# Kernel tuning notes

Measured on AMD Instinct MI355X. Metric: run time of the kernel, lower is better.

The kernel has to match this reference:

```python
import jax, jax.numpy as jnp
import numpy as np

N_NODES = 50000
N_EDGES = 1000000
NEG_SLOPE = 0.2


def _gat_layer(x, W, attn_l, attn_r, bias, src, dst, n_nodes):
    """DGL-style GATConv. x:[N,Fin], W:[H*D,Fin], attn_l/attn_r:[H,D], bias:[H*D].
    Returns [N, H*D] after ReLU activation (flattened heads)."""
    H, D = attn_l.shape
    h = (x @ W.T).reshape(n_nodes, H, D)                    # [N,H,D]
    el = jnp.sum(h * attn_l[None], axis=-1)                 # [N,H]
    er = jnp.sum(h * attn_r[None], axis=-1)                 # [N,H]
    e = jax.nn.leaky_relu(el[src] + er[dst], NEG_SLOPE)     # [E,H]
    # edge softmax over incoming edges per destination node
    emax = jax.ops.segment_max(e, dst, num_segments=n_nodes)  # [N,H]
    emax = jnp.where(jnp.isfinite(emax), emax, 0.0)
    a = jnp.exp(e - emax[dst])                               # [E,H]
    denom = jax.ops.segment_sum(a, dst, num_segments=n_nodes)  # [N,H]
    alpha = a / denom[dst]                                   # [E,H]
    msg = alpha[:, :, None] * h[src]                         # [E,H,D]
    out = jax.ops.segment_sum(msg, dst, num_segments=n_nodes)  # [N,H,D]
    out = out + bias.reshape(1, H, D)
    out = jax.nn.relu(out)
    return out.reshape(n_nodes, H * D)


def setup_inputs() -> dict:
    key = jax.random.key(0)
    ks = jax.random.split(key, 16)
    features = jax.random.normal(ks[0], (N_NODES, 25), dtype=jnp.float32)
    src = jax.random.randint(ks[1], (N_EDGES,), 0, N_NODES, dtype=jnp.int32)
    dst = jax.random.randint(ks[2], (N_EDGES,), 0, N_NODES, dtype=jnp.int32)

    def glorot(k, shape, fan):
        return jax.random.normal(k, shape, dtype=jnp.float32) * (1.0 / np.sqrt(fan))

    # layer 1: in=25, out=10, heads=4
    W1 = glorot(ks[3], (40, 25), 25)
    al1 = glorot(ks[4], (4, 10), 10)
    ar1 = glorot(ks[5], (4, 10), 10)
    b1 = jnp.zeros((40,), dtype=jnp.float32)
    # layer 2: in=40, out=25, heads=4
    W2 = glorot(ks[6], (100, 40), 40)
    al2 = glorot(ks[7], (4, 25), 25)
    ar2 = glorot(ks[8], (4, 25), 25)
    b2 = jnp.zeros((100,), dtype=jnp.float32)
    # layer 3: in=100, out=50, heads=1
    W3 = glorot(ks[9], (50, 100), 100)
    al3 = glorot(ks[10], (1, 50), 50)
    ar3 = glorot(ks[11], (1, 50), 50)
    b3 = jnp.zeros((50,), dtype=jnp.float32)
    # final fc: 50 -> 93
    fc_w = glorot(ks[12], (93, 50), 50)
    fc_b = jnp.zeros((93,), dtype=jnp.float32)
    return {
        "features": features, "src": src, "dst": dst,
        "W1": W1, "al1": al1, "ar1": ar1, "b1": b1,
        "W2": W2, "al2": al2, "ar2": ar2, "b2": b2,
        "W3": W3, "al3": al3, "ar3": ar3, "b3": b3,
        "fc_w": fc_w, "fc_b": fc_b,
    }


def reference(features, src, dst,
              W1, al1, ar1, b1,
              W2, al2, ar2, b2,
              W3, al3, ar3, b3,
              fc_w, fc_b):
    n = features.shape[0]
    h = _gat_layer(features, W1, al1, ar1, b1, src, dst, n)   # [N,40]
    h = _gat_layer(h, W2, al2, ar2, b2, src, dst, n)          # [N,100]
    h = _gat_layer(h, W3, al3, ar3, b3, src, dst, n)          # [N,50]
    return h @ fc_w.T + fc_b                                  # [N,93]
```

## Files before the change

### kernel.cpp

```cpp
#include <hip/hip_runtime.h>
#include <hip/hip_bf16.h>

#ifndef NEG_SLOPE
#define NEG_SLOPE 0.2f
#endif

static inline int cdiv(long long a, long long b) { return (int)((a + b - 1) / b); }

__device__ __forceinline__ float lrelu(float v) { return v > 0.f ? v : NEG_SLOPE * v; }

__global__ void k_prep(const float* __restrict__ W1, const float* __restrict__ al1,
                       const float* __restrict__ ar1, const float* __restrict__ W2,
                       const float* __restrict__ al2, const float* __restrict__ ar2,
                       const float* __restrict__ W3, const float* __restrict__ al3,
                       const float* __restrict__ ar3, float* __restrict__ wx1,
                       float* __restrict__ wx2, float* __restrict__ wx3,
                       const int* __restrict__ dst, int* __restrict__ deg, int n_edges) {
    if (blockIdx.x < 3) {
        int b = blockIdx.x;
        const float *W, *al, *ar;
        float* wx;
        int FIN, FOUT, H, D;
        if (b == 0) { W = W1; al = al1; ar = ar1; wx = wx1; FIN = 25; FOUT = 40; H = 4; D = 10; }
        else if (b == 1) { W = W2; al = al2; ar = ar2; wx = wx2; FIN = 40; FOUT = 100; H = 4; D = 25; }
        else { W = W3; al = al3; ar = ar3; wx = wx3; FIN = 100; FOUT = 50; H = 1; D = 50; }
        for (int i = threadIdx.x; i < FOUT * FIN; i += blockDim.x) wx[i] = W[i];
        for (int i = threadIdx.x; i < 2 * H * FIN; i += blockDim.x) {
            int row = i / FIN, k = i % FIN;
            int h = row % H, isR = row / H;
            const float* a = isR ? ar : al;
            float s = 0.f;
            for (int d = 0; d < D; ++d) s += W[(h * D + d) * FIN + k] * a[h * D + d];
            wx[(FOUT + isR * H + h) * FIN + k] = s;
        }
    } else {
        int e = (blockIdx.x - 3) * blockDim.x + threadIdx.x;
        if (e < n_edges) atomicAdd(&deg[dst[e]], 1);
    }
}

__global__ void k_scan_block(const int* __restrict__ deg, int* __restrict__ incl,
                             int* __restrict__ blocksum, int n) {
    __shared__ int tmp[256];
    int t = threadIdx.x;
    int i = blockIdx.x * 256 + t;
    int v = (i < n) ? deg[i] : 0;
    tmp[t] = v;
    __syncthreads();
    for (int off = 1; off < 256; off <<= 1) {
        int add = (t >= off) ? tmp[t - off] : 0;
        __syncthreads();
        tmp[t] += add;
        __syncthreads();
    }
    if (i < n) incl[i] = tmp[t];
    if (t == 255) blocksum[blockIdx.x] = tmp[t];
}

__global__ void k_scan_top(const int* __restrict__ blocksum, int* __restrict__ blockoff, int nb) {
    __shared__ int tmp[256];
    int t = threadIdx.x;
    int base = 0;
    for (int c = 0; c < nb; c += 256) {
        int i = c + t;
        int v = (i < nb) ? blocksum[i] : 0;
        tmp[t] = v;
        __syncthreads();
        for (int off = 1; off < 256; off <<= 1) {
            int add = (t >= off) ? tmp[t - off] : 0;
            __syncthreads();
            tmp[t] += add;
            __syncthreads();
        }
        if (i < nb) blockoff[i] = base + tmp[t] - v;
        base += tmp[255];
        __syncthreads();
    }
}

__global__ void k_scan_finalize(const int* __restrict__ incl, const int* __restrict__ deg,
                                const int* __restrict__ blockoff, int* __restrict__ rowptr,
                                int n, int n_edges) {
    int i = blockIdx.x * blockDim.x + threadIdx.x;
    if (i < n) rowptr[i] = incl[i] - deg[i] + blockoff[i / 256];
    if (i == 0) rowptr[n] = n_edges;
}

template <int FIN, int FOUT, int H>
__global__ void k_linear(const float* __restrict__ x, const float* __restrict__ wx,
                         float* __restrict__ h, float* __restrict__ el, float* __restrict__ er,
                         int n_nodes) {
    constexpr int FOUTE = FOUT + 2 * H;
    __shared__ float Ws[FIN * FOUTE];
    for (int i = threadIdx.x; i < FIN * FOUTE; i += blockDim.x) {
        int f = i / FIN, k = i % FIN;
        Ws[k * FOUTE + f] = wx[i];
    }
    __syncthreads();
    int idx = blockIdx.x * blockDim.x + threadIdx.x;
    if (idx >= n_nodes * FOUTE) return;
    int n = idx / FOUTE, f = idx % FOUTE;
    const float* __restrict__ xr = x + (long long)n * FIN;
    float acc = 0.f;
#pragma unroll
    for (int k = 0; k < FIN; ++k) acc += xr[k] * Ws[k * FOUTE + f];
    if (f < FOUT) h[(long long)n * FOUT + f] = acc;
    else if (f < FOUT + H) el[n * H + (f - FOUT)] = acc;
    else er[n * H + (f - FOUT - H)] = acc;
}

__global__ void k_fill(const int* __restrict__ src, const int* __restrict__ dst,
                       const int* __restrict__ rowptr, int* __restrict__ cursor,
                       int* __restrict__ csr_src, int n_edges) {
    int e = blockIdx.x * blockDim.x + threadIdx.x;
    if (e >= n_edges) return;
    int d = dst[e];
    int pos = atomicAdd(&cursor[d], 1);
    csr_src[rowptr[d] + pos] = src[e];
}

__global__ void k_sort_wave(const int* __restrict__ rowptr, int* __restrict__ csr_src,
                            int n_nodes) {
    int wid = (blockIdx.x * blockDim.x + threadIdx.x) >> 6;
    int lane = threadIdx.x & 63;
    if (wid >= n_nodes) return;
    int s0 = rowptr[wid], e0 = rowptr[wid + 1];
    int d = e0 - s0;
    if (d <= 1) return;
    if (d <= 64) {
        int v = (lane < d) ? csr_src[s0 + lane] : 0x7FFFFFFF;
        int rank = 0;
        for (int k = 0; k < d; ++k) {
            int vk = __shfl(v, k);
            rank += (vk < v || (vk == v && k < lane)) ? 1 : 0;
        }
        if (lane < d) csr_src[s0 + rank] = v;
    } else if (lane == 0) {
        for (int a = s0 + 1; a < e0; ++a) {
            int key = csr_src[a];
            int b = a - 1;
            while (b >= s0 && csr_src[b] > key) { csr_src[b + 1] = csr_src[b]; --b; }
            csr_src[b + 1] = key;
        }
    }
}

template <int FOUT, int H, int D, int EB>
__global__ void k_node_gather(const int* __restrict__ rowptr, const int* __restrict__ csr_src,
                              const float* __restrict__ el, const float* __restrict__ er,
                              const float* __restrict__ h, const float* __restrict__ bias,
                              float* __restrict__ xout, int n_nodes) {
    constexpr int NF = (FOUT + 63) / 64;
    int wid = (blockIdx.x * blockDim.x + threadIdx.x) >> 6;
    int lane = threadIdx.x & 63;
    if (wid >= n_nodes) return;
    int start = rowptr[wid], end = rowptr[wid + 1];

    const int eidx = lane / H;
    const int hh_c = lane % H;
    const float er_c = er[wid * H + hh_c];

    float acc[NF];
    int f_i[NF], hh_i[NF];
#pragma unroll
    for (int r = 0; r < NF; ++r) {
        int f = lane + r * 64;
        f_i[r] = f;
        hh_i[r] = (f < FOUT) ? (f / D) : 0;
        acc[r] = 0.f;
    }
    float den_acc = 0.f;

    if (start < end) {
        int j0 = start;
        int nb = end - j0;
        if (nb > EB) nb = EB;
        int s_c = csr_src[j0 + (eidx < nb ? eidx : 0)];
        float e_c = el[s_c * H + hh_c];

        while (true) {
            int j1 = j0 + nb;
            int nbn = end - j1;
            if (nbn > EB) nbn = EB;
            int s_n = 0;
            float e_n = 0.f;
            if (nbn > 0) {
                s_n = csr_src[j1 + (eidx < nbn ? eidx : 0)];
                e_n = el[s_n * H + hh_c];
            }
            float p_c = expf(lrelu(e_c + er_c));
            float pd = (eidx < nb) ? p_c : 0.f;
#pragma unroll
            for (int st = H; st < 64; st <<= 1) pd += __shfl_xor(pd, st);
            den_acc += pd;

            float hv[EB * NF];
#pragma unroll
            for (int e = 0; e < EB; ++e) {
                if (e < nb) {
                    int s = __shfl(s_c, e * H);
                    const float* __restrict__ hrow = h + (long long)s * FOUT;
#pragma unroll
                    for (int r = 0; r < NF; ++r)
                        if (f_i[r] < FOUT) hv[e * NF + r] = hrow[f_i[r]];
                }
            }
#pragma unroll
            for (int e = 0; e < EB; ++e) {
                if (e < nb) {
#pragma unroll
                    for (int r = 0; r < NF; ++r) {
                        float p = __shfl(p_c, e * H + hh_i[r]);
                        if (f_i[r] < FOUT) acc[r] += p * hv[e * NF + r];
                    }
                }
            }
            if (nbn <= 0) break;
            j0 = j1;
            nb = nbn;
            s_c = s_n;
            e_c = e_n;
        }
    }

    float den_r[NF];
#pragma unroll
    for (int r = 0; r < NF; ++r) den_r[r] = __shfl(den_acc, hh_i[r]);
#pragma unroll
    for (int r = 0; r < NF; ++r) {
        if (f_i[r] < FOUT) {
            float val;
            if (end > start) val = acc[r] / den_r[r] + bias[f_i[r]];
            else val = bias[f_i[r]];
            xout[(long long)wid * FOUT + f_i[r]] = val > 0.f ? val : 0.f;
        }
    }
}

template <int FIN, int FOUT>
__global__ void k_fc(const float* __restrict__ x, const float* __restrict__ W,
                     const float* __restrict__ b, float* __restrict__ out, int n_nodes) {
    __shared__ float Ws[FIN * FOUT];
    for (int i = threadIdx.x; i < FIN * FOUT; i += blockDim.x) {
        int f = i / FIN, k = i % FIN;
        Ws[k * FOUT + f] = W[i];
    }
    __syncthreads();
    int idx = blockIdx.x * blockDim.x + threadIdx.x;
    if (idx >= n_nodes * FOUT) return;
    int n = idx / FOUT, f = idx % FOUT;
    const float* __restrict__ xr = x + (long long)n * FIN;
    float acc = b[f];
#pragma unroll
    for (int k = 0; k < FIN; ++k) acc += xr[k] * Ws[k * FOUT + f];
    out[idx] = acc;
}

template <int FIN, int FOUT, int H, int D, int EB>
static void gat_layer(const float* x, const float* wext, const float* bias, const int* rowptr,
                      const int* csr_src, int n_nodes, float* bufH, float* el, float* er,
                      float* xnext, hipStream_t stream) {
    constexpr int FOUTE = FOUT + 2 * H;
    k_linear<FIN, FOUT, H><<<cdiv((long long)n_nodes * FOUTE, 256), 256, 0, stream>>>(
        x, wext, bufH, el, er, n_nodes);
    k_node_gather<FOUT, H, D, EB><<<cdiv((long long)n_nodes * 64, 256), 256, 0, stream>>>(
        rowptr, csr_src, el, er, bufH, bias, xnext, n_nodes);
}

extern "C" void kernel_launch(void* const* d_in, const int* in_sizes, int n_in,
                              void* d_out, int out_size, void* d_ws, size_t ws_size,
                              hipStream_t stream) {
    const float* features = (const float*)d_in[0];
    const int* src = (const int*)d_in[1];
    const int* dst = (const int*)d_in[2];
    const float* W1 = (const float*)d_in[3];
    const float* al1 = (const float*)d_in[4];
    const float* ar1 = (const float*)d_in[5];
    const float* b1 = (const float*)d_in[6];
    const float* W2 = (const float*)d_in[7];
    const float* al2 = (const float*)d_in[8];
    const float* ar2 = (const float*)d_in[9];
    const float* b2 = (const float*)d_in[10];
    const float* W3 = (const float*)d_in[11];
    const float* al3 = (const float*)d_in[12];
    const float* ar3 = (const float*)d_in[13];
    const float* b3 = (const float*)d_in[14];
    const float* fc_w = (const float*)d_in[15];
    const float* fc_b = (const float*)d_in[16];

    const int n_nodes = in_sizes[0] / 25;
    const int n_edges = in_sizes[1];
    const int nblocks_nodes = cdiv(n_nodes, 256);

    char* ws = (char*)d_ws;
    size_t off = 0;
    auto alloc = [&](size_t bytes) {
        char* p = ws + off;
        off += (bytes + 255) & ~(size_t)255;
        return p;
    };
    float* bufA = (float*)alloc((size_t)n_nodes * 100 * sizeof(float));
    float* bufH = (float*)alloc((size_t)n_nodes * 100 * sizeof(float));
    float* el = (float*)alloc((size_t)n_nodes * 4 * sizeof(float));
    float* er = (float*)alloc((size_t)n_nodes * 4 * sizeof(float));
    int* degcur = (int*)alloc((size_t)2 * n_nodes * sizeof(int));
    int* deg = degcur;
    int* cursor = degcur + n_nodes;
    int* incl = (int*)alloc((size_t)n_nodes * sizeof(int));
    int* blocksum = (int*)alloc((size_t)nblocks_nodes * sizeof(int));
    int* blockoff = (int*)alloc((size_t)nblocks_nodes * sizeof(int));
    int* rowptr = (int*)alloc((size_t)(n_nodes + 1) * sizeof(int));
    int* csr_src = (int*)alloc((size_t)n_edges * sizeof(int));
    float* wx1 = (float*)alloc((size_t)48 * 25 * sizeof(float));
    float* wx2 = (float*)alloc((size_t)108 * 40 * sizeof(float));
    float* wx3 = (float*)alloc((size_t)52 * 100 * sizeof(float));
    (void)ws_size;

    hipMemsetAsync(degcur, 0, (size_t)2 * n_nodes * sizeof(int), stream);
    k_prep<<<3 + cdiv(n_edges, 256), 256, 0, stream>>>(W1, al1, ar1, W2, al2, ar2, W3, al3,
                                                       ar3, wx1, wx2, wx3, dst, deg, n_edges);
    k_scan_block<<<nblocks_nodes, 256, 0, stream>>>(deg, incl, blocksum, n_nodes);
    k_scan_top<<<1, 256, 0, stream>>>(blocksum, blockoff, nblocks_nodes);
    k_scan_finalize<<<cdiv(n_nodes + 1, 256), 256, 0, stream>>>(incl, deg, blockoff, rowptr,
                                                                n_nodes, n_edges);
    k_fill<<<cdiv(n_edges, 256), 256, 0, stream>>>(src, dst, rowptr, cursor, csr_src, n_edges);
    k_sort_wave<<<cdiv((long long)n_nodes * 64, 256), 256, 0, stream>>>(rowptr, csr_src,
                                                                        n_nodes);

    gat_layer<25, 40, 4, 10, 16>(features, wx1, b1, rowptr, csr_src, n_nodes, bufH, el, er,
                                 bufA, stream);
    gat_layer<40, 100, 4, 25, 16>(bufA, wx2, b2, rowptr, csr_src, n_nodes, bufH, el, er,
                                  bufA, stream);
    gat_layer<100, 50, 1, 50, 32>(bufA, wx3, b3, rowptr, csr_src, n_nodes, bufH, el, er,
                                  bufA, stream);

    k_fc<50, 93><<<cdiv((long long)n_nodes * 93, 256), 256, 0, stream>>>(
        bufA, fc_w, fc_b, (float*)d_out, n_nodes);
}
```

Baseline: 512.6 us.

## Fuse each layer's gather with the next layer's linear projection and final FC

Each gather kernel now keeps the aggregated node row in shared memory and multiplies it by the next layer's extended weight matrix, which it also stages in shared memory. It writes h, el and er for the next layer, or the final FC output for the last layer. This removes two standalone linear kernels and the FC kernel, along with the global round trips of the intermediate activations. In exchange each block loads the full weight matrix into shared memory, and each lane runs a serial dot product of up to 100 terms per output column. The shared memory footprint may also lower occupancy.

```diff
diff --git a/kernel.cpp b/kernel.cpp
--- a/kernel.cpp
+++ b/kernel.cpp
@@ -145,14 +145,27 @@
     }
 }
 
-template <int FOUT, int H, int D, int EB>
-__global__ void k_node_gather(const int* __restrict__ rowptr, const int* __restrict__ csr_src,
-                              const float* __restrict__ el, const float* __restrict__ er,
-                              const float* __restrict__ h, const float* __restrict__ bias,
-                              float* __restrict__ xout, int n_nodes) {
+template <int FOUT, int H, int D, int EB, int FOUTE2, int FOUT2, int H2, int OUT_MODE>
+__global__ void k_gather_linear(const int* __restrict__ rowptr, const int* __restrict__ csr_src,
+                                const float* __restrict__ el, const float* __restrict__ er,
+                                const float* __restrict__ h, const float* __restrict__ bias,
+                                const float* __restrict__ wx2, const float* __restrict__ fcb,
+                                float* __restrict__ h2, float* __restrict__ el2,
+                                float* __restrict__ er2, int n_nodes) {
     constexpr int NF = (FOUT + 63) / 64;
+    constexpr int FIN2 = FOUT;
+    constexpr int NR2 = (FOUTE2 + 63) / 64;
+    __shared__ float Ws[FIN2 * FOUTE2];
+    __shared__ float xrow[4][FIN2];
+    for (int i = threadIdx.x; i < FIN2 * FOUTE2; i += blockDim.x) {
+        int f = i / FIN2, k = i % FIN2;
+        Ws[k * FOUTE2 + f] = wx2[i];
+    }
+    __syncthreads();
+
     int wid = (blockIdx.x * blockDim.x + threadIdx.x) >> 6;
     int lane = threadIdx.x & 63;
+    int wv = threadIdx.x >> 6;
     if (wid >= n_nodes) return;
     int start = rowptr[wid], end = rowptr[wid + 1];
 
@@ -232,39 +245,25 @@
             float val;
             if (end > start) val = acc[r] / den_r[r] + bias[f_i[r]];
             else val = bias[f_i[r]];
-            xout[(long long)wid * FOUT + f_i[r]] = val > 0.f ? val : 0.f;
-        }
-    }
-}
-
-template <int FIN, int FOUT>
-__global__ void k_fc(const float* __restrict__ x, const float* __restrict__ W,
-                     const float* __restrict__ b, float* __restrict__ out, int n_nodes) {
-    __shared__ float Ws[FIN * FOUT];
-    for (int i = threadIdx.x; i < FIN * FOUT; i += blockDim.x) {
-        int f = i / FIN, k = i % FIN;
-        Ws[k * FOUT + f] = W[i];
-    }
-    __syncthreads();
-    int idx = blockIdx.x * blockDim.x + threadIdx.x;
-    if (idx >= n_nodes * FOUT) return;
-    int n = idx / FOUT, f = idx % FOUT;
-    const float* __restrict__ xr = x + (long long)n * FIN;
-    float acc = b[f];
-#pragma unroll
-    for (int k = 0; k < FIN; ++k) acc += xr[k] * Ws[k * FOUT + f];
-    out[idx] = acc;
-}
-
-template <int FIN, int FOUT, int H, int D, int EB>
-static void gat_layer(const float* x, const float* wext, const float* bias, const int* rowptr,
-                      const int* csr_src, int n_nodes, float* bufH, float* el, float* er,
-                      float* xnext, hipStream_t stream) {
-    constexpr int FOUTE = FOUT + 2 * H;
-    k_linear<FIN, FOUT, H><<<cdiv((long long)n_nodes * FOUTE, 256), 256, 0, stream>>>(
-        x, wext, bufH, el, er, n_nodes);
-    k_node_gather<FOUT, H, D, EB><<<cdiv((long long)n_nodes * 64, 256), 256, 0, stream>>>(
-        rowptr, csr_src, el, er, bufH, bias, xnext, n_nodes);
+            xrow[wv][f_i[r]] = val > 0.f ? val : 0.f;
+        }
+    }
+
+#pragma unroll
+    for (int r2 = 0; r2 < NR2; ++r2) {
+        int f2 = lane + r2 * 64;
+        if (f2 < FOUTE2) {
+            float a2 = (OUT_MODE == 1) ? fcb[f2] : 0.f;
+            for (int k = 0; k < FIN2; ++k) a2 += xrow[wv][k] * Ws[k * FOUTE2 + f2];
+            if (OUT_MODE == 1) {
+                h2[(long long)wid * FOUTE2 + f2] = a2;
+            } else {
+                if (f2 < FOUT2) h2[(long long)wid * FOUT2 + f2] = a2;
+                else if (f2 < FOUT2 + H2) el2[wid * H2 + (f2 - FOUT2)] = a2;
+                else er2[wid * H2 + (f2 - FOUT2 - H2)] = a2;
+            }
+        }
+    }
 }
 
 extern "C" void kernel_launch(void* const* d_in, const int* in_sizes, int n_in,
@@ -291,6 +290,7 @@
     const int n_nodes = in_sizes[0] / 25;
     const int n_edges = in_sizes[1];
     const int nblocks_nodes = cdiv(n_nodes, 256);
+    const int gather_blocks = cdiv((long long)n_nodes * 64, 256);
 
     char* ws = (char*)d_ws;
     size_t off = 0;
@@ -299,10 +299,12 @@
         off += (bytes + 255) & ~(size_t)255;
         return p;
     };
-    float* bufA = (float*)alloc((size_t)n_nodes * 100 * sizeof(float));
-    float* bufH = (float*)alloc((size_t)n_nodes * 100 * sizeof(float));
-    float* el = (float*)alloc((size_t)n_nodes * 4 * sizeof(float));
-    float* er = (float*)alloc((size_t)n_nodes * 4 * sizeof(float));
+    float* hA = (float*)alloc((size_t)n_nodes * 100 * sizeof(float));
+    float* hB = (float*)alloc((size_t)n_nodes * 100 * sizeof(float));
+    float* el0 = (float*)alloc((size_t)n_nodes * 4 * sizeof(float));
+    float* er0 = (float*)alloc((size_t)n_nodes * 4 * sizeof(float));
+    float* el1 = (float*)alloc((size_t)n_nodes * 4 * sizeof(float));
+    float* er1 = (float*)alloc((size_t)n_nodes * 4 * sizeof(float));
     int* degcur = (int*)alloc((size_t)2 * n_nodes * sizeof(int));
     int* deg = degcur;
     int* cursor = degcur + n_nodes;
@@ -324,16 +326,18 @@
     k_scan_finalize<<<cdiv(n_nodes + 1, 256), 256, 0, stream>>>(incl, deg, blockoff, rowptr,
                                                                 n_nodes, n_edges);
     k_fill<<<cdiv(n_edges, 256), 256, 0, stream>>>(src, dst, rowptr, cursor, csr_src, n_edges);
-    k_sort_wave<<<cdiv((long long)n_nodes * 64, 256), 256, 0, stream>>>(rowptr, csr_src,
-                                                                        n_nodes);
-
-    gat_layer<25, 40, 4, 10, 16>(features, wx1, b1, rowptr, csr_src, n_nodes, bufH, el, er,
-                                 bufA, stream);
-    gat_layer<40, 100, 4, 25, 16>(bufA, wx2, b2, rowptr, csr_src, n_nodes, bufH, el, er,
-                                  bufA, stream);
-    gat_layer<100, 50, 1, 50, 32>(bufA, wx3, b3, rowptr, csr_src, n_nodes, bufH, el, er,
-                                  bufA, stream);
-
-    k_fc<50, 93><<<cdiv((long long)n_nodes * 93, 256), 256, 0, stream>>>(
-        bufA, fc_w, fc_b, (float*)d_out, n_nodes);
-}
+    k_sort_wave<<<gather_blocks, 256, 0, stream>>>(rowptr, csr_src, n_nodes);
+
+    k_linear<25, 40, 4><<<cdiv((long long)n_nodes * 48, 256), 256, 0, stream>>>(
+        features, wx1, hA, el0, er0, n_nodes);
+
+    k_gather_linear<40, 4, 10, 16, 108, 100, 4, 0><<<gather_blocks, 256, 0, stream>>>(
+        rowptr, csr_src, el0, er0, hA, b1, wx2, nullptr, hB, el1, er1, n_nodes);
+
+    k_gather_linear<100, 4, 25, 16, 52, 50, 1, 0><<<gather_blocks, 256, 0, stream>>>(
+        rowptr, csr_src, el1, er1, hB, b2, wx3, nullptr, hA, el0, er0, n_nodes);
+
+    k_gather_linear<50, 1, 50, 32, 93, 93, 0, 1><<<gather_blocks, 256, 0, stream>>>(
+        rowptr, csr_src, el0, er0, hA, b3, fc_w, fc_b, (float*)d_out, nullptr, nullptr,
+        n_nodes);
+}
```

Measured after the change: 509.7 us. No clear change (-0.6%).
